# Kernel optimization log

Hardware: AMD Instinct MI355X
Metric: run time of the kernel (lower is better)

## Reference

```python
import jax, jax.numpy as jnp
import numpy as np

B = 8192      # sessions
L = 64        # tokens per session
T = B * L     # total tokens
H = 128       # hidden_size
MAX_LEN = 64  # position_emb has MAX_LEN+1 rows


def setup_inputs() -> dict:
    key = jax.random.key(0)
    ks = jax.random.split(key, 10)
    s1 = 1.0 / np.sqrt(H)
    s2 = 1.0 / np.sqrt(2 * H)
    hidden = jax.random.normal(ks[0], (T, H), jnp.float32)
    seq_len = jnp.full((B,), L, dtype=jnp.int32)
    # reversed positions 1..L within each session (<= MAX_LEN)
    reverse_pos = jnp.tile(jnp.arange(L, 0, -1, dtype=jnp.int32), B)
    return {
        "hidden": hidden,
        "pos_table": jax.random.normal(ks[1], (MAX_LEN + 1, H), jnp.float32) * 0.02,
        "W_pos_w": jax.random.normal(ks[2], (H, 2 * H), jnp.float32) * s2,
        "W_pos_b": jax.random.normal(ks[3], (H,), jnp.float32) * s2,
        "W1_w": jax.random.normal(ks[4], (H, H), jnp.float32) * s1,
        "W1_b": jax.random.normal(ks[5], (H,), jnp.float32) * s1,
        "W2_w": jax.random.normal(ks[6], (H, H), jnp.float32) * s1,
        "W2_b": jax.random.normal(ks[7], (H,), jnp.float32) * s1,
        "q_w": jax.random.normal(ks[8], (1, H), jnp.float32) * s1,
        "q_b": jax.random.normal(ks[9], (1,), jnp.float32) * s1,
        "seq_len": seq_len,
        "reverse_pos": reverse_pos,
    }


def reference(hidden, pos_table, W_pos_w, W_pos_b, W1_w, W1_b, W2_w, W2_b,
              q_w, q_b, seq_len, reverse_pos):
    Bn = seq_len.shape[0]
    Tn = hidden.shape[0]
    # token -> session id (replaces the python split loop)
    seg = jnp.repeat(jnp.arange(Bn), seq_len, total_repeat_length=Tn)  # [T]
    # per-session mean, broadcast back to tokens (v_mean_repeat_concat)
    mean = jax.ops.segment_sum(hidden, seg, num_segments=Bn) \
        / seq_len[:, None].astype(hidden.dtype)                        # [B,H]
    mean_rep = mean[seg]                                               # [T,H]
    pos_emb = pos_table[reverse_pos]                                   # [T,H]
    pos_hidden = jnp.tanh(
        jnp.concatenate([hidden, pos_emb], axis=-1) @ W_pos_w.T + W_pos_b
    )                                                                  # [T,H]
    gate = jax.nn.sigmoid(mean_rep @ W1_w.T + W1_b + pos_hidden @ W2_w.T + W2_b)
    alpha = gate @ q_w.T + q_b                                         # [T,1]
    # per-session sum of alpha-weighted tokens (h_s)
    return jax.ops.segment_sum(alpha * hidden, seg, num_segments=Bn)   # [B,H]
```

## Files before the change

kernel.cpp:

```cpp
#include <hip/hip_runtime.h>
#include <hip/hip_bf16.h>

typedef unsigned short u16;
typedef __bf16 bf16x8 __attribute__((ext_vector_type(8)));
typedef float  f32x4  __attribute__((ext_vector_type(4)));

__device__ __forceinline__ unsigned pk2(float a, float b) {
    __hip_bfloat162 h = __float22bfloat162_rn(make_float2(a, b));
    unsigned u; __builtin_memcpy(&u, &h, 4);
    return u;
}
__device__ __forceinline__ u16 f2b1(float f) { return (u16)(pk2(f, f) & 0xFFFFu); }

#define MFMA __builtin_amdgcn_mfma_f32_16x16x32_bf16

__global__ __launch_bounds__(128) void prep_kernel(
    const float* __restrict__ pos_table, const float* __restrict__ Wpw,
    const float* __restrict__ Wpb, const float* __restrict__ W2,
    float* __restrict__ ppK, u16* __restrict__ wb1, u16* __restrict__ wb2)
{
    const int b = blockIdx.x, t = threadIdx.x;
    if (b < 65) {
        const float4* pr = (const float4*)(pos_table + b * 128);
        const float4* wr = (const float4*)(Wpw + t * 256 + 128);
        float acc = Wpb[t];
        #pragma unroll
        for (int k = 0; k < 32; ++k) {
            const float4 p = pr[k], wv = wr[k];
            acc += p.x * wv.x + p.y * wv.y + p.z * wv.z + p.w * wv.w;
        }
        ppK[b * 128 + t] = acc * 2.885390081777927f;
    } else {
        const int j = b - 65;
        const int off = (((j >> 4) * 4 + (t >> 5)) * 16 + (j & 15)) * 32 + (t & 31);
        wb1[off] = f2b1(Wpw[j * 256 + t]);
        wb2[off] = f2b1(W2[j * 128 + t]);
    }
}

__global__ __launch_bounds__(256, 2) void fused_kernel(
    const float* __restrict__ hidden, const int* __restrict__ rpos,
    const float* __restrict__ W1, const float* __restrict__ W1b,
    const float* __restrict__ W2b, const float* __restrict__ qw,
    const float* __restrict__ qb, const float* __restrict__ ppK,
    const u16* __restrict__ wb1g, const u16* __restrict__ wb2g,
    float* __restrict__ out)
{
    __shared__ __align__(16) u16 hbf[128 * 136];
    __shared__ float meanv[256];
    __shared__ float g1s[256];
    __shared__ float qws[128];
    __shared__ float alphas[128];
    __shared__ int   rps[128];

    const int tid = threadIdx.x;
    const int blk = blockIdx.x;
    const int w = tid >> 6;
    const int l = tid & 63;
    const int c = l & 15;
    const int g = l >> 4;
    const int R = 32 * w;
    const float* hsrc = hidden + (size_t)blk * (128 * 128);

    meanv[tid] = 0.f;
    if (tid < 128) { rps[tid] = rpos[blk * 128 + tid]; qws[tid] = qw[tid]; }
    __syncthreads();

    {
        float4 ms0 = {0.f, 0.f, 0.f, 0.f}, ms1 = {0.f, 0.f, 0.f, 0.f};
        #pragma unroll
        for (int i = 0; i < 16; ++i) {
            const int i4 = tid + i * 256;
            const float4 v = ((const float4*)hsrc)[i4];
            const int e = i4 * 4, row = e >> 7, col = e & 127;
            uint2 st; st.x = pk2(v.x, v.y); st.y = pk2(v.z, v.w);
            *(uint2*)&hbf[row * 136 + col] = st;
            if (i < 8) { ms0.x += v.x; ms0.y += v.y; ms0.z += v.z; ms0.w += v.w; }
            else       { ms1.x += v.x; ms1.y += v.y; ms1.z += v.z; ms1.w += v.w; }
        }
        ms0.x += __shfl_xor(ms0.x, 32, 64); ms0.y += __shfl_xor(ms0.y, 32, 64);
        ms0.z += __shfl_xor(ms0.z, 32, 64); ms0.w += __shfl_xor(ms0.w, 32, 64);
        ms1.x += __shfl_xor(ms1.x, 32, 64); ms1.y += __shfl_xor(ms1.y, 32, 64);
        ms1.z += __shfl_xor(ms1.z, 32, 64); ms1.w += __shfl_xor(ms1.w, 32, 64);
        if ((l & 32) == 0) {
            const int mc = (tid * 4) & 127;
            atomicAdd(&meanv[mc],           ms0.x); atomicAdd(&meanv[mc + 1],       ms0.y);
            atomicAdd(&meanv[mc + 2],       ms0.z); atomicAdd(&meanv[mc + 3],       ms0.w);
            atomicAdd(&meanv[128 + mc],     ms1.x); atomicAdd(&meanv[128 + mc + 1], ms1.y);
            atomicAdd(&meanv[128 + mc + 2], ms1.z); atomicAdd(&meanv[128 + mc + 3], ms1.w);
        }
    }
    __syncthreads();

    {
        const int col = tid & 127, s = tid >> 7;
        const float4* wr = (const float4*)(W1 + col * 128);
        const float4* mv = (const float4*)(meanv + s * 128);
        float acc = 0.f;
        #pragma unroll 8
        for (int k4 = 0; k4 < 32; ++k4) {
            const float4 wv = wr[k4], m4 = mv[k4];
            acc += m4.x * wv.x + m4.y * wv.y + m4.z * wv.z + m4.w * wv.w;
        }
        g1s[tid] = W1b[col] + W2b[col] + acc * (1.f / 64.f);
    }

    bf16x8 af[2][4];
    #pragma unroll
    for (int m = 0; m < 2; ++m)
        #pragma unroll
        for (int kk = 0; kk < 4; ++kk)
            af[m][kk] = *(const bf16x8*)&hbf[(R + 16 * m + c) * 136 + kk * 32 + g * 8];

    int pko[2][4];
    #pragma unroll
    for (int m = 0; m < 2; ++m)
        #pragma unroll
        for (int r = 0; r < 4; ++r)
            pko[m][r] = rps[R + 16 * m + 4 * g + r] * 128 + c;

    {
        const u16* wb1p = wb1g + c * 32 + g * 8;
        bf16x8 bf[8][4];
        #pragma unroll
        for (int n = 0; n < 8; ++n)
            #pragma unroll
            for (int kk = 0; kk < 4; ++kk)
                bf[n][kk] = *(const bf16x8*)(wb1p + n * 2048 + kk * 512);
        const float K2 = 2.885390081777927f;
        #pragma unroll
        for (int n = 0; n < 8; ++n) {
            float ppv[2][4];
            #pragma unroll
            for (int m = 0; m < 2; ++m)
                #pragma unroll
                for (int r = 0; r < 4; ++r)
                    ppv[m][r] = ppK[pko[m][r] + 16 * n];
            f32x4 acc[2] = {};
            #pragma unroll
            for (int kk = 0; kk < 4; ++kk) {
                acc[0] = MFMA(af[0][kk], bf[n][kk], acc[0], 0, 0, 0);
                acc[1] = MFMA(af[1][kk], bf[n][kk], acc[1], 0, 0, 0);
            }
            #pragma unroll
            for (int m = 0; m < 2; ++m)
                #pragma unroll
                for (int r = 0; r < 4; ++r) {
                    const float arg = fmaf(acc[m][r], K2, ppv[m][r]);
                    const float e2 = __builtin_amdgcn_exp2f(arg);
                    const float rc = __builtin_amdgcn_rcpf(e2 + 1.f);
                    hbf[(R + 16 * m + 4 * g + r) * 136 + 16 * n + c] =
                        f2b1(fmaf(-2.f, rc, 1.f));
                }
        }
    }

    bf16x8 af2[2][4];
    #pragma unroll
    for (int m = 0; m < 2; ++m)
        #pragma unroll
        for (int kk = 0; kk < 4; ++kk)
            af2[m][kk] = *(const bf16x8*)&hbf[(R + 16 * m + c) * 136 + kk * 32 + g * 8];

    bf16x8 bf2[8][4];
    {
        const u16* wb2p = wb2g + c * 32 + g * 8;
        #pragma unroll
        for (int n = 0; n < 8; ++n)
            #pragma unroll
            for (int kk = 0; kk < 4; ++kk)
                bf2[n][kk] = *(const bf16x8*)(wb2p + n * 2048 + kk * 512);
    }

    __syncthreads();

    {
        const float K1 = 1.4426950408889634f;
        const int sw = w >> 1;
        float prt[2][4] = {};
        #pragma unroll
        for (int n = 0; n < 8; ++n) {
            f32x4 acc[2] = {};
            #pragma unroll
            for (int kk = 0; kk < 4; ++kk) {
                acc[0] = MFMA(af2[0][kk], bf2[n][kk], acc[0], 0, 0, 0);
                acc[1] = MFMA(af2[1][kk], bf2[n][kk], acc[1], 0, 0, 0);
            }
            const float gv = -K1 * g1s[sw * 128 + 16 * n + c];
            const float qv = qws[16 * n + c];
            #pragma unroll
            for (int m = 0; m < 2; ++m)
                #pragma unroll
                for (int r = 0; r < 4; ++r) {
                    const float arg = fmaf(acc[m][r], -K1, gv);
                    const float e2 = __builtin_amdgcn_exp2f(arg);
                    const float rc = __builtin_amdgcn_rcpf(e2 + 1.f);
                    prt[m][r] = fmaf(rc, qv, prt[m][r]);
                }
        }
        #pragma unroll
        for (int msk = 1; msk <= 8; msk <<= 1)
            #pragma unroll
            for (int m = 0; m < 2; ++m)
                #pragma unroll
                for (int r = 0; r < 4; ++r)
                    prt[m][r] += __shfl_xor(prt[m][r], msk, 64);
        if (c == 0) {
            const float qbv = qb[0];
            #pragma unroll
            for (int m = 0; m < 2; ++m)
                #pragma unroll
                for (int r = 0; r < 4; ++r)
                    alphas[R + 16 * m + 4 * g + r] = prt[m][r] + qbv;
        }
    }
    __syncthreads();

    {
        const int h = tid & 127, p = tid >> 7;
        const float* hs = hsrc + p * (64 * 128) + h;
        float a8[8];
        #pragma unroll
        for (int j = 0; j < 8; ++j) a8[j] = 0.f;
        #pragma unroll
        for (int t0 = 0; t0 < 8; ++t0) {
            float v[8], al[8];
            #pragma unroll
            for (int j = 0; j < 8; ++j) {
                v[j]  = hs[(t0 * 8 + j) * 128];
                al[j] = alphas[64 * p + t0 * 8 + j];
            }
            #pragma unroll
            for (int j = 0; j < 8; ++j) a8[j] = fmaf(al[j], v[j], a8[j]);
        }
        const float accf = ((a8[0] + a8[1]) + (a8[2] + a8[3]))
                         + ((a8[4] + a8[5]) + (a8[6] + a8[7]));
        out[(size_t)blk * 256 + tid] = accf;
    }
}

extern "C" void kernel_launch(void* const* d_in, const int* in_sizes, int n_in,
                              void* d_out, int out_size, void* d_ws, size_t ws_size,
                              hipStream_t stream)
{
    const float* hidden    = (const float*)d_in[0];
    const float* pos_table = (const float*)d_in[1];
    const float* Wpw       = (const float*)d_in[2];
    const float* Wpb       = (const float*)d_in[3];
    const float* W1w       = (const float*)d_in[4];
    const float* W1b       = (const float*)d_in[5];
    const float* W2w       = (const float*)d_in[6];
    const float* W2b       = (const float*)d_in[7];
    const float* qw        = (const float*)d_in[8];
    const float* qb        = (const float*)d_in[9];
    const int*   rpos      = (const int*)d_in[11];
    float* out = (float*)d_out;

    const int B = in_sizes[10];

    char* wsb = (char*)d_ws;
    float* ppK = (float*)wsb;
    u16* wb1   = (u16*)(wsb + 33280);
    u16* wb2   = (u16*)(wsb + 33280 + 32768);

    prep_kernel<<<193, 128, 0, stream>>>(pos_table, Wpw, Wpb, W2w,
                                         ppK, wb1, wb2);
    fused_kernel<<<B / 2, 256, 0, stream>>>(hidden, rpos, W1w, W1b, W2b, qw, qb,
                                            ppK, wb1, wb2, out);
}
```

Baseline: 479.8 us.

## Make fused kernel persistent and prefetch next pair's hidden tile into registers

The fused kernel becomes a grid-stride persistent loop over session pairs, with at most 512 blocks. While the current pair is computed, each thread loads the next pair's 64 KB hidden tile into registers (16 float4 per thread), so global loads overlap with compute. The B-fragment weights are now loaded per n-iteration instead of being held in large register arrays, and the W1 dot uses two accumulators. This costs many more live registers, which may spill or limit occupancy under launch_bounds(256,2), and the persistent grid relies on enough resident waves to hide latency.

```diff
diff --git a/kernel.cpp b/kernel.cpp
--- a/kernel.cpp
+++ b/kernel.cpp
@@ -44,198 +44,218 @@
     const float* __restrict__ W2b, const float* __restrict__ qw,
     const float* __restrict__ qb, const float* __restrict__ ppK,
     const u16* __restrict__ wb1g, const u16* __restrict__ wb2g,
-    float* __restrict__ out)
+    float* __restrict__ out, const int npairs)
 {
     __shared__ __align__(16) u16 hbf[128 * 136];
     __shared__ float meanv[256];
     __shared__ float g1s[256];
     __shared__ float qws[128];
     __shared__ float alphas[128];
-    __shared__ int   rps[128];
 
     const int tid = threadIdx.x;
-    const int blk = blockIdx.x;
     const int w = tid >> 6;
     const int l = tid & 63;
     const int c = l & 15;
     const int g = l >> 4;
     const int R = 32 * w;
-    const float* hsrc = hidden + (size_t)blk * (128 * 128);
-
-    meanv[tid] = 0.f;
-    if (tid < 128) { rps[tid] = rpos[blk * 128 + tid]; qws[tid] = qw[tid]; }
-    __syncthreads();
-
+
+    if (tid < 128) qws[tid] = qw[tid];
+
+    int pair = blockIdx.x;
+    float4 pf[16];
     {
-        float4 ms0 = {0.f, 0.f, 0.f, 0.f}, ms1 = {0.f, 0.f, 0.f, 0.f};
-        #pragma unroll
-        for (int i = 0; i < 16; ++i) {
-            const int i4 = tid + i * 256;
-            const float4 v = ((const float4*)hsrc)[i4];
-            const int e = i4 * 4, row = e >> 7, col = e & 127;
-            uint2 st; st.x = pk2(v.x, v.y); st.y = pk2(v.z, v.w);
-            *(uint2*)&hbf[row * 136 + col] = st;
-            if (i < 8) { ms0.x += v.x; ms0.y += v.y; ms0.z += v.z; ms0.w += v.w; }
-            else       { ms1.x += v.x; ms1.y += v.y; ms1.z += v.z; ms1.w += v.w; }
-        }
-        ms0.x += __shfl_xor(ms0.x, 32, 64); ms0.y += __shfl_xor(ms0.y, 32, 64);
-        ms0.z += __shfl_xor(ms0.z, 32, 64); ms0.w += __shfl_xor(ms0.w, 32, 64);
-        ms1.x += __shfl_xor(ms1.x, 32, 64); ms1.y += __shfl_xor(ms1.y, 32, 64);
-        ms1.z += __shfl_xor(ms1.z, 32, 64); ms1.w += __shfl_xor(ms1.w, 32, 64);
-        if ((l & 32) == 0) {
-            const int mc = (tid * 4) & 127;
-            atomicAdd(&meanv[mc],           ms0.x); atomicAdd(&meanv[mc + 1],       ms0.y);
-            atomicAdd(&meanv[mc + 2],       ms0.z); atomicAdd(&meanv[mc + 3],       ms0.w);
-            atomicAdd(&meanv[128 + mc],     ms1.x); atomicAdd(&meanv[128 + mc + 1], ms1.y);
-            atomicAdd(&meanv[128 + mc + 2], ms1.z); atomicAdd(&meanv[128 + mc + 3], ms1.w);
-        }
+        const float4* hp = (const float4*)(hidden + (size_t)pair * 16384);
+        #pragma unroll
+        for (int i = 0; i < 16; ++i) pf[i] = hp[tid + i * 256];
     }
-    __syncthreads();
-
-    {
-        const int col = tid & 127, s = tid >> 7;
-        const float4* wr = (const float4*)(W1 + col * 128);
-        const float4* mv = (const float4*)(meanv + s * 128);
-        float acc = 0.f;
-        #pragma unroll 8
-        for (int k4 = 0; k4 < 32; ++k4) {
-            const float4 wv = wr[k4], m4 = mv[k4];
-            acc += m4.x * wv.x + m4.y * wv.y + m4.z * wv.z + m4.w * wv.w;
-        }
-        g1s[tid] = W1b[col] + W2b[col] + acc * (1.f / 64.f);
-    }
-
-    bf16x8 af[2][4];
-    #pragma unroll
-    for (int m = 0; m < 2; ++m)
-        #pragma unroll
-        for (int kk = 0; kk < 4; ++kk)
-            af[m][kk] = *(const bf16x8*)&hbf[(R + 16 * m + c) * 136 + kk * 32 + g * 8];
-
-    int pko[2][4];
-    #pragma unroll
-    for (int m = 0; m < 2; ++m)
-        #pragma unroll
-        for (int r = 0; r < 4; ++r)
-            pko[m][r] = rps[R + 16 * m + 4 * g + r] * 128 + c;
-
-    {
-        const u16* wb1p = wb1g + c * 32 + g * 8;
-        bf16x8 bf[8][4];
-        #pragma unroll
-        for (int n = 0; n < 8; ++n)
+
+    for (; pair < npairs; pair += gridDim.x) {
+        const float* hsrc = hidden + (size_t)pair * 16384;
+
+        meanv[tid] = 0.f;
+        __syncthreads();
+
+        {
+            float4 ms0 = {0.f, 0.f, 0.f, 0.f}, ms1 = {0.f, 0.f, 0.f, 0.f};
+            #pragma unroll
+            for (int i = 0; i < 16; ++i) {
+                const int i4 = tid + i * 256;
+                const float4 v = pf[i];
+                const int e = i4 * 4, row = e >> 7, col = e & 127;
+                uint2 st; st.x = pk2(v.x, v.y); st.y = pk2(v.z, v.w);
+                *(uint2*)&hbf[row * 136 + col] = st;
+                if (i < 8) { ms0.x += v.x; ms0.y += v.y; ms0.z += v.z; ms0.w += v.w; }
+                else       { ms1.x += v.x; ms1.y += v.y; ms1.z += v.z; ms1.w += v.w; }
+            }
+            ms0.x += __shfl_xor(ms0.x, 32, 64); ms0.y += __shfl_xor(ms0.y, 32, 64);
+            ms0.z += __shfl_xor(ms0.z, 32, 64); ms0.w += __shfl_xor(ms0.w, 32, 64);
+            ms1.x += __shfl_xor(ms1.x, 32, 64); ms1.y += __shfl_xor(ms1.y, 32, 64);
+            ms1.z += __shfl_xor(ms1.z, 32, 64); ms1.w += __shfl_xor(ms1.w, 32, 64);
+            if ((l & 32) == 0) {
+                const int mc = (tid * 4) & 127;
+                atomicAdd(&meanv[mc],           ms0.x); atomicAdd(&meanv[mc + 1],       ms0.y);
+                atomicAdd(&meanv[mc + 2],       ms0.z); atomicAdd(&meanv[mc + 3],       ms0.w);
+                atomicAdd(&meanv[128 + mc],     ms1.x); atomicAdd(&meanv[128 + mc + 1], ms1.y);
+                atomicAdd(&meanv[128 + mc + 2], ms1.z); atomicAdd(&meanv[128 + mc + 3], ms1.w);
+            }
+        }
+        __syncthreads();
+
+        {
+            const int nxt = pair + gridDim.x;
+            if (nxt < npairs) {
+                const float4* hp = (const float4*)(hidden + (size_t)nxt * 16384);
+                #pragma unroll
+                for (int i = 0; i < 16; ++i) pf[i] = hp[tid + i * 256];
+            }
+        }
+
+        {
+            const int col = tid & 127, s = tid >> 7;
+            const float4* wr = (const float4*)(W1 + col * 128);
+            const float4* mv = (const float4*)(meanv + s * 128);
+            float a0 = 0.f, a1 = 0.f;
+            #pragma unroll 8
+            for (int k4 = 0; k4 < 32; k4 += 2) {
+                const float4 w0 = wr[k4], m0 = mv[k4];
+                const float4 w1v = wr[k4 + 1], m1 = mv[k4 + 1];
+                a0 += m0.x * w0.x + m0.y * w0.y + m0.z * w0.z + m0.w * w0.w;
+                a1 += m1.x * w1v.x + m1.y * w1v.y + m1.z * w1v.z + m1.w * w1v.w;
+            }
+            g1s[tid] = W1b[col] + W2b[col] + (a0 + a1) * (1.f / 64.f);
+        }
+
+        bf16x8 af[2][4];
+        #pragma unroll
+        for (int m = 0; m < 2; ++m)
             #pragma unroll
             for (int kk = 0; kk < 4; ++kk)
-                bf[n][kk] = *(const bf16x8*)(wb1p + n * 2048 + kk * 512);
-        const float K2 = 2.885390081777927f;
-        #pragma unroll
-        for (int n = 0; n < 8; ++n) {
-            float ppv[2][4];
-            #pragma unroll
-            for (int m = 0; m < 2; ++m)
-                #pragma unroll
-                for (int r = 0; r < 4; ++r)
-                    ppv[m][r] = ppK[pko[m][r] + 16 * n];
-            f32x4 acc[2] = {};
-            #pragma unroll
-            for (int kk = 0; kk < 4; ++kk) {
-                acc[0] = MFMA(af[0][kk], bf[n][kk], acc[0], 0, 0, 0);
-                acc[1] = MFMA(af[1][kk], bf[n][kk], acc[1], 0, 0, 0);
-            }
-            #pragma unroll
-            for (int m = 0; m < 2; ++m)
-                #pragma unroll
-                for (int r = 0; r < 4; ++r) {
-                    const float arg = fmaf(acc[m][r], K2, ppv[m][r]);
-                    const float e2 = __builtin_amdgcn_exp2f(arg);
-                    const float rc = __builtin_amdgcn_rcpf(e2 + 1.f);
-                    hbf[(R + 16 * m + 4 * g + r) * 136 + 16 * n + c] =
-                        f2b1(fmaf(-2.f, rc, 1.f));
+                af[m][kk] = *(const bf16x8*)&hbf[(R + 16 * m + c) * 136 + kk * 32 + g * 8];
+
+        int pko[2][4];
+        #pragma unroll
+        for (int m = 0; m < 2; ++m)
+            #pragma unroll
+            for (int r = 0; r < 4; ++r)
+                pko[m][r] = rpos[pair * 128 + R + 16 * m + 4 * g + r] * 128 + c;
+
+        {
+            const u16* wb1p = wb1g + c * 32 + g * 8;
+            const float K2 = 2.885390081777927f;
+            #pragma unroll
+            for (int n = 0; n < 8; ++n) {
+                float ppv[2][4];
+                #pragma unroll
+                for (int m = 0; m < 2; ++m)
+                    #pragma unroll
+                    for (int r = 0; r < 4; ++r)
+                        ppv[m][r] = ppK[pko[m][r] + 16 * n];
+                bf16x8 b0 = *(const bf16x8*)(wb1p + n * 2048);
+                bf16x8 b1 = *(const bf16x8*)(wb1p + n * 2048 + 512);
+                bf16x8 b2 = *(const bf16x8*)(wb1p + n * 2048 + 1024);
+                bf16x8 b3 = *(const bf16x8*)(wb1p + n * 2048 + 1536);
+                f32x4 acc[2] = {};
+                acc[0] = MFMA(af[0][0], b0, acc[0], 0, 0, 0);
+                acc[1] = MFMA(af[1][0], b0, acc[1], 0, 0, 0);
+                acc[0] = MFMA(af[0][1], b1, acc[0], 0, 0, 0);
+                acc[1] = MFMA(af[1][1], b1, acc[1], 0, 0, 0);
+                acc[0] = MFMA(af[0][2], b2, acc[0], 0, 0, 0);
+                acc[1] = MFMA(af[1][2], b2, acc[1], 0, 0, 0);
+                acc[0] = MFMA(af[0][3], b3, acc[0], 0, 0, 0);
+                acc[1] = MFMA(af[1][3], b3, acc[1], 0, 0, 0);
+                #pragma unroll
+                for (int m = 0; m < 2; ++m)
+                    #pragma unroll
+                    for (int r = 0; r < 4; ++r) {
+                        const float arg = fmaf(acc[m][r], K2, ppv[m][r]);
+                        const float e2 = __builtin_amdgcn_exp2f(arg);
+                        const float rc = __builtin_amdgcn_rcpf(e2 + 1.f);
+                        hbf[(R + 16 * m + 4 * g + r) * 136 + 16 * n + c] =
+                            f2b1(fmaf(-2.f, rc, 1.f));
+                    }
+            }
+        }
+
+        bf16x8 af2[2][4];
+        #pragma unroll
+        for (int m = 0; m < 2; ++m)
+            #pragma unroll
+            for (int kk = 0; kk < 4; ++kk)
+                af2[m][kk] = *(const bf16x8*)&hbf[(R + 16 * m + c) * 136 + kk * 32 + g * 8];
+
+        __syncthreads();
+
+        {
+            const u16* wb2p = wb2g + c * 32 + g * 8;
+            const float K1 = 1.4426950408889634f;
+            const int sw = w >> 1;
+            float prt[2][4] = {};
+            #pragma unroll
+            for (int n = 0; n < 8; ++n) {
+                bf16x8 b0 = *(const bf16x8*)(wb2p + n * 2048);
+                bf16x8 b1 = *(const bf16x8*)(wb2p + n * 2048 + 512);
+                bf16x8 b2 = *(const bf16x8*)(wb2p + n * 2048 + 1024);
+                bf16x8 b3 = *(const bf16x8*)(wb2p + n * 2048 + 1536);
+                f32x4 acc[2] = {};
+                acc[0] = MFMA(af2[0][0], b0, acc[0], 0, 0, 0);
+                acc[1] = MFMA(af2[1][0], b0, acc[1], 0, 0, 0);
+                acc[0] = MFMA(af2[0][1], b1, acc[0], 0, 0, 0);
+                acc[1] = MFMA(af2[1][1], b1, acc[1], 0, 0, 0);
+                acc[0] = MFMA(af2[0][2], b2, acc[0], 0, 0, 0);
+                acc[1] = MFMA(af2[1][2], b2, acc[1], 0, 0, 0);
+                acc[0] = MFMA(af2[0][3], b3, acc[0], 0, 0, 0);
+                acc[1] = MFMA(af2[1][3], b3, acc[1], 0, 0, 0);
+                const float gv = -K1 * g1s[sw * 128 + 16 * n + c];
+                const float qv = qws[16 * n + c];
+                #pragma unroll
+                for (int m = 0; m < 2; ++m)
+                    #pragma unroll
+                    for (int r = 0; r < 4; ++r) {
+                        const float arg = fmaf(acc[m][r], -K1, gv);
+                        const float e2 = __builtin_amdgcn_exp2f(arg);
+                        const float rc = __builtin_amdgcn_rcpf(e2 + 1.f);
+                        prt[m][r] = fmaf(rc, qv, prt[m][r]);
+                    }
+            }
+            #pragma unroll
+            for (int msk = 1; msk <= 8; msk <<= 1)
+                #pragma unroll
+                for (int m = 0; m < 2; ++m)
+                    #pragma unroll
+                    for (int r = 0; r < 4; ++r)
+                        prt[m][r] += __shfl_xor(prt[m][r], msk, 64);
+            if (c == 0) {
+                const float qbv = qb[0];
+                #pragma unroll
+                for (int m = 0; m < 2; ++m)
+                    #pragma unroll
+                    for (int r = 0; r < 4; ++r)
+                        alphas[R + 16 * m + 4 * g + r] = prt[m][r] + qbv;
+            }
+        }
+        __syncthreads();
+
+        {
+            const int h = tid & 127, p = tid >> 7;
+            const float* hs = hsrc + p * (64 * 128) + h;
+            float a8[8];
+            #pragma unroll
+            for (int j = 0; j < 8; ++j) a8[j] = 0.f;
+            #pragma unroll
+            for (int t0 = 0; t0 < 4; ++t0) {
+                float v[16], al[16];
+                #pragma unroll
+                for (int j = 0; j < 16; ++j) {
+                    v[j]  = hs[(t0 * 16 + j) * 128];
+                    al[j] = alphas[64 * p + t0 * 16 + j];
                 }
-        }
-    }
-
-    bf16x8 af2[2][4];
-    #pragma unroll
-    for (int m = 0; m < 2; ++m)
-        #pragma unroll
-        for (int kk = 0; kk < 4; ++kk)
-            af2[m][kk] = *(const bf16x8*)&hbf[(R + 16 * m + c) * 136 + kk * 32 + g * 8];
-
-    bf16x8 bf2[8][4];
-    {
-        const u16* wb2p = wb2g + c * 32 + g * 8;
-        #pragma unroll
-        for (int n = 0; n < 8; ++n)
-            #pragma unroll
-            for (int kk = 0; kk < 4; ++kk)
-                bf2[n][kk] = *(const bf16x8*)(wb2p + n * 2048 + kk * 512);
-    }
-
-    __syncthreads();
-
-    {
-        const float K1 = 1.4426950408889634f;
-        const int sw = w >> 1;
-        float prt[2][4] = {};
-        #pragma unroll
-        for (int n = 0; n < 8; ++n) {
-            f32x4 acc[2] = {};
-            #pragma unroll
-            for (int kk = 0; kk < 4; ++kk) {
-                acc[0] = MFMA(af2[0][kk], bf2[n][kk], acc[0], 0, 0, 0);
-                acc[1] = MFMA(af2[1][kk], bf2[n][kk], acc[1], 0, 0, 0);
-            }
-            const float gv = -K1 * g1s[sw * 128 + 16 * n + c];
-            const float qv = qws[16 * n + c];
-            #pragma unroll
-            for (int m = 0; m < 2; ++m)
-                #pragma unroll
-                for (int r = 0; r < 4; ++r) {
-                    const float arg = fmaf(acc[m][r], -K1, gv);
-                    const float e2 = __builtin_amdgcn_exp2f(arg);
-                    const float rc = __builtin_amdgcn_rcpf(e2 + 1.f);
-                    prt[m][r] = fmaf(rc, qv, prt[m][r]);
-                }
-        }
-        #pragma unroll
-        for (int msk = 1; msk <= 8; msk <<= 1)
-            #pragma unroll
-            for (int m = 0; m < 2; ++m)
-                #pragma unroll
-                for (int r = 0; r < 4; ++r)
-                    prt[m][r] += __shfl_xor(prt[m][r], msk, 64);
-        if (c == 0) {
-            const float qbv = qb[0];
-            #pragma unroll
-            for (int m = 0; m < 2; ++m)
-                #pragma unroll
-                for (int r = 0; r < 4; ++r)
-                    alphas[R + 16 * m + 4 * g + r] = prt[m][r] + qbv;
-        }
-    }
-    __syncthreads();
-
-    {
-        const int h = tid & 127, p = tid >> 7;
-        const float* hs = hsrc + p * (64 * 128) + h;
-        float a8[8];
-        #pragma unroll
-        for (int j = 0; j < 8; ++j) a8[j] = 0.f;
-        #pragma unroll
-        for (int t0 = 0; t0 < 8; ++t0) {
-            float v[8], al[8];
-            #pragma unroll
-            for (int j = 0; j < 8; ++j) {
-                v[j]  = hs[(t0 * 8 + j) * 128];
-                al[j] = alphas[64 * p + t0 * 8 + j];
-            }
-            #pragma unroll
-            for (int j = 0; j < 8; ++j) a8[j] = fmaf(al[j], v[j], a8[j]);
-        }
-        const float accf = ((a8[0] + a8[1]) + (a8[2] + a8[3]))
-                         + ((a8[4] + a8[5]) + (a8[6] + a8[7]));
-        out[(size_t)blk * 256 + tid] = accf;
+                #pragma unroll
+                for (int j = 0; j < 16; ++j) a8[j & 7] = fmaf(al[j], v[j], a8[j & 7]);
+            }
+            const float accf = ((a8[0] + a8[1]) + (a8[2] + a8[3]))
+                             + ((a8[4] + a8[5]) + (a8[6] + a8[7]));
+            out[(size_t)pair * 256 + tid] = accf;
+        }
     }
 }
 
@@ -257,6 +277,8 @@
     float* out = (float*)d_out;
 
     const int B = in_sizes[10];
+    const int npairs = B / 2;
+    const int grid = npairs < 512 ? npairs : 512;
 
     char* wsb = (char*)d_ws;
     float* ppK = (float*)wsb;
@@ -265,6 +287,6 @@
 
     prep_kernel<<<193, 128, 0, stream>>>(pos_table, Wpw, Wpb, W2w,
                                          ppK, wb1, wb2);
-    fused_kernel<<<B / 2, 256, 0, stream>>>(hidden, rpos, W1w, W1b, W2b, qw, qb,
-                                            ppK, wb1, wb2, out);
-}
+    fused_kernel<<<grid, 256, 0, stream>>>(hidden, rpos, W1w, W1b, W2b, qw, qb,
+                                           ppK, wb1, wb2, out, npairs);
+}
```

After: 633.4 us. 32.0% more time.
